# Performance work log

Measured on AMD Instinct MI355X. Metric: run time of the kernel, lower is better.

## Reference

```python
import jax, jax.numpy as jnp
import numpy as np

N = 50000
E = 625000
IN_NODE = 128
IN_EDGE = 64
H = 128
OUT = 112
L = 3


def setup_inputs() -> dict:
    key = jax.random.key(0)
    ks = jax.random.split(key, 16)
    s = lambda fan_in: 1.0 / np.sqrt(fan_in)
    inp = {
        "x": jax.random.normal(ks[0], (N, IN_NODE), jnp.float32),
        "edge_attr": jax.random.normal(ks[1], (E, IN_EDGE), jnp.float32),
        "edge_index": jax.random.randint(ks[2], (2, E), 0, N, jnp.int32),
        # encoders
        "node_W": jax.random.uniform(ks[3], (IN_NODE, H), jnp.float32, -s(IN_NODE), s(IN_NODE)),
        "node_b": jnp.zeros((H,), jnp.float32),
        "edge_W": jax.random.uniform(ks[4], (IN_EDGE, H), jnp.float32, -s(IN_EDGE), s(IN_EDGE)),
        "edge_b": jnp.zeros((H,), jnp.float32),
        # per-layer GINConv MLP params, stacked over layers
        "W1": jax.random.uniform(ks[5], (L, H, 2 * H), jnp.float32, -s(H), s(H)),
        "b1": jnp.zeros((L, 2 * H), jnp.float32),
        "W2": jax.random.uniform(ks[6], (L, 2 * H, H), jnp.float32, -s(2 * H), s(2 * H)),
        "b2": jnp.zeros((L, H), jnp.float32),
        "eps": jnp.zeros((L,), jnp.float32),
        # output head
        "lin_W": jax.random.uniform(ks[7], (H, OUT), jnp.float32, -s(H), s(H)),
        "lin_b": jnp.zeros((OUT,), jnp.float32),
    }
    return inp


def reference(x, edge_attr, edge_index, node_W, node_b, edge_W, edge_b,
              W1, b1, W2, b2, eps, lin_W, lin_b):
    src = edge_index[0]  # x_j gather indices (source nodes)
    dst = edge_index[1]  # scatter targets
    n = x.shape[0]

    x = x @ node_W + node_b                 # [N, H]
    ea = edge_attr @ edge_W + edge_b        # [E, H]

    # in-degree for mean aggregation (clamped at 1, zero-degree -> 0 agg)
    deg = jax.ops.segment_sum(jnp.ones((src.shape[0],), x.dtype), dst, num_segments=n)
    inv_deg = 1.0 / jnp.maximum(deg, 1.0)   # [N]

    for l in range(L):
        msg = x[src] + ea                                    # [E, H]
        agg = jax.ops.segment_sum(msg, dst, num_segments=n)  # [N, H]
        agg = agg * inv_deg[:, None]                         # mean
        h = (1.0 + eps[l]) * x + agg
        h = jax.nn.relu(h @ W1[l] + b1[l]) @ W2[l] + b2[l]   # GIN MLP
        x = jax.nn.relu(h)                                   # dropout is identity in eval

    return x @ lin_W + lin_b                 # [N, OUT]
```

## Files before the change

kernel.cpp:

```cpp
#include <hip/hip_runtime.h>


typedef unsigned short u16;
typedef unsigned int   u32;

using short8 = __attribute__((ext_vector_type(8))) short;
using f32x4  = __attribute__((ext_vector_type(4))) float;
using f32x2  = __attribute__((ext_vector_type(2))) float;

__device__ __forceinline__ float b2f(u16 u) {
  union { u32 i; float f; } v; v.i = ((u32)u) << 16; return v.f;
}
__device__ __forceinline__ u16 f2b(float f) {
  union { float f; u32 i; } v; v.f = f;
  u32 i = v.i;
  return (u16)((i + 0x7FFFu + ((i >> 16) & 1u)) >> 16);
}

__global__ void sniff_kernel(const u16* __restrict__ xu, int* __restrict__ flag) {
  __shared__ int cnt;
  if (threadIdx.x == 0) cnt = 0;
  __syncthreads();
  int c = 0;
  for (int i = threadIdx.x; i < 1024; i += 256) {
    int e = (xu[i] >> 7) & 0xFF;
    if (e >= 100 && e <= 140) c++;
  }
  atomicAdd(&cnt, c);
  __syncthreads();
  if (threadIdx.x == 0) *flag = (cnt >= 820) ? 1 : 0;
}

__global__ void cvt_bf16_kernel(const void* __restrict__ src, u16* __restrict__ dst,
                                int n, const int* __restrict__ flag) {
  int i = blockIdx.x * 256 + threadIdx.x;
  if (i >= n) return;
  if (*flag) dst[i] = ((const u16*)src)[i];
  else       dst[i] = f2b(((const float*)src)[i]);
}

__global__ void transpose_cvt_kernel(const void* __restrict__ src, u16* __restrict__ dst,
                                     int K, int N, int total, const int* __restrict__ flag) {
  int i = blockIdx.x * 256 + threadIdx.x;
  if (i >= total) return;
  int kn = K * N;
  int l = i / kn, r = i - l * kn;
  int k = r / N, n = r - k * N;
  u16 v = (*flag) ? ((const u16*)src)[i] : f2b(((const float*)src)[i]);
  dst[(size_t)l * kn + n * K + k] = v;
}

struct BiasJobs { const void* src[6]; float* dst[6]; int len[6]; };
__global__ void cvt_bias_kernel(BiasJobs j, const int* __restrict__ flag) {
  int b = blockIdx.x;
  int isbf = *flag;
  for (int i = threadIdx.x; i < j.len[b]; i += 256) {
    j.dst[b][i] = isbf ? b2f(((const u16*)j.src[b])[i]) : ((const float*)j.src[b])[i];
  }
}

__global__ void deg_kernel(const int* __restrict__ dst, int* __restrict__ deg, int e) {
  int i = blockIdx.x * 256 + threadIdx.x;
  if (i < e) atomicAdd(&deg[dst[i]], 1);
}

__global__ void scanA_kernel(const int* __restrict__ deg, int* __restrict__ rowptr,
                             float* __restrict__ invdeg, int* __restrict__ btot, int n) {
  __shared__ int wsum[4];
  int tid = threadIdx.x, lane = tid & 63, wid = tid >> 6;
  int i = blockIdx.x * 256 + tid;
  int v = (i < n) ? deg[i] : 0;
  int incl = v;
  #pragma unroll
  for (int off = 1; off < 64; off <<= 1) {
    int t = __shfl_up(incl, off, 64);
    if (lane >= off) incl += t;
  }
  if (lane == 63) wsum[wid] = incl;
  __syncthreads();
  int woff = 0;
  for (int w = 0; w < wid; ++w) woff += wsum[w];
  if (i < n) {
    rowptr[i] = woff + incl - v;
    invdeg[i] = 1.0f / fmaxf((float)v, 1.0f);
  }
  if (tid == 255) btot[blockIdx.x] = woff + incl;
}

__global__ void scanB_kernel(int* __restrict__ btot, int nb) {
  __shared__ int wsum[4];
  int tid = threadIdx.x, lane = tid & 63, wid = tid >> 6;
  int v = (tid < nb) ? btot[tid] : 0;
  int incl = v;
  #pragma unroll
  for (int off = 1; off < 64; off <<= 1) {
    int t = __shfl_up(incl, off, 64);
    if (lane >= off) incl += t;
  }
  if (lane == 63) wsum[wid] = incl;
  __syncthreads();
  int woff = 0;
  for (int w = 0; w < wid; ++w) woff += wsum[w];
  if (tid < nb) btot[tid] = woff + incl - v;
}

__global__ void scanC_kernel(int* __restrict__ rowptr, const int* __restrict__ btot,
                             int n, int e) {
  int i = blockIdx.x * 256 + threadIdx.x;
  if (i < n) rowptr[i] += btot[blockIdx.x];
  if (i == 0) rowptr[n] = e;
}

__global__ void fill_kernel(const int* __restrict__ src, const int* __restrict__ dst,
                            const int* __restrict__ rowptr, int* __restrict__ fillc,
                            int* __restrict__ csr_src, int* __restrict__ csr_eid, int e) {
  int i = blockIdx.x * 256 + threadIdx.x;
  if (i < e) {
    int d = dst[i];
    int p = rowptr[d] + atomicAdd(&fillc[d], 1);
    csr_src[p] = src[i];
    csr_eid[p] = i;
  }
}

__global__ __launch_bounds__(256) void sattr_gather_kernel(
    const void* __restrict__ ea, const int* __restrict__ rowptr,
    const int* __restrict__ csr_eid, float* __restrict__ sattr,
    int nnodes, const int* __restrict__ flag) {
  int tid = threadIdx.x, lane = tid & 63, wid = tid >> 6;
  int node = blockIdx.x * 4 + wid;
  if (node >= nnodes) return;
  int hl = lane >> 5, l32 = lane & 31;
  int r0 = rowptr[node], r1 = rowptr[node + 1];
  int isbf = *flag;
  float s0 = 0.f, s1 = 0.f;
  if (isbf) {
    const u32* ea32 = (const u32*)ea;
    int j = r0 + hl;
    for (; j + 6 < r1; j += 8) {
      int e0 = csr_eid[j], e1 = csr_eid[j + 2], e2 = csr_eid[j + 4], e3 = csr_eid[j + 6];
      u32 v0 = ea32[(size_t)e0 * 32 + l32];
      u32 v1 = ea32[(size_t)e1 * 32 + l32];
      u32 v2 = ea32[(size_t)e2 * 32 + l32];
      u32 v3 = ea32[(size_t)e3 * 32 + l32];
      s0 += b2f((u16)(v0 & 0xffff)) + b2f((u16)(v1 & 0xffff)) +
            b2f((u16)(v2 & 0xffff)) + b2f((u16)(v3 & 0xffff));
      s1 += b2f((u16)(v0 >> 16)) + b2f((u16)(v1 >> 16)) +
            b2f((u16)(v2 >> 16)) + b2f((u16)(v3 >> 16));
    }
    for (; j < r1; j += 2) {
      u32 v = ea32[(size_t)csr_eid[j] * 32 + l32];
      s0 += b2f((u16)(v & 0xffff));
      s1 += b2f((u16)(v >> 16));
    }
  } else {
    const f32x2* eaf = (const f32x2*)ea;
    int j = r0 + hl;
    for (; j + 6 < r1; j += 8) {
      f32x2 v0 = eaf[(size_t)csr_eid[j] * 32 + l32];
      f32x2 v1 = eaf[(size_t)csr_eid[j + 2] * 32 + l32];
      f32x2 v2 = eaf[(size_t)csr_eid[j + 4] * 32 + l32];
      f32x2 v3 = eaf[(size_t)csr_eid[j + 6] * 32 + l32];
      s0 += v0.x + v1.x + v2.x + v3.x;
      s1 += v0.y + v1.y + v2.y + v3.y;
    }
    for (; j < r1; j += 2) {
      f32x2 v = eaf[(size_t)csr_eid[j] * 32 + l32];
      s0 += v.x; s1 += v.y;
    }
  }
  s0 += __shfl_xor(s0, 32, 64);
  s1 += __shfl_xor(s1, 32, 64);
  if (hl == 0) {
    f32x2 o; o.x = s0; o.y = s1;
    *reinterpret_cast<f32x2*>(&sattr[(size_t)node * 64 + l32 * 2]) = o;
  }
}

template <int K, int N, int ACT, int MODE>
__global__ __launch_bounds__(256) void gemm_kernel(
    const void* __restrict__ Av, const u16* __restrict__ WT,
    const float* __restrict__ bias, void* __restrict__ Cv, int M,
    const int* __restrict__ flag, const float* __restrict__ rowscale,
    const int* __restrict__ degp) {
  constexpr int KC = 64;
  constexpr int KCP = KC + 8;
  constexpr int NF = N / 16;
  constexpr int NV = N * KC / 8;
  static_assert(K % KC == 0 && N % 16 == 0, "dims");
  __shared__ u16 WS[N * KCP];

  int tid = threadIdx.x, lane = tid & 63, wid = tid >> 6;
  int lane16 = lane & 15, lh = lane >> 4;
  int row0 = blockIdx.x * 128 + wid * 32;
  int arow0 = row0 + lane16;       if (arow0 >= M) arow0 = M - 1;
  int arow1 = row0 + 16 + lane16;  if (arow1 >= M) arow1 = M - 1;

  f32x4 acc[2][NF];
  #pragma unroll
  for (int rb = 0; rb < 2; ++rb)
    #pragma unroll
    for (int i = 0; i < NF; ++i) acc[rb][i] = (f32x4){0.f, 0.f, 0.f, 0.f};

  for (int kc0 = 0; kc0 < K; kc0 += KC) {
    #pragma unroll
    for (int v = tid; v < NV; v += 256) {
      int n = v >> 3, k8 = (v & 7) << 3;
      *reinterpret_cast<short8*>(&WS[n * KCP + k8]) =
          *reinterpret_cast<const short8*>(&WT[(size_t)n * K + kc0 + k8]);
    }
    __syncthreads();
    #pragma unroll
    for (int ks = 0; ks < KC; ks += 32) {
      short8 a0, a1;
      if (MODE == 2) {
        const float* Af0 = (const float*)Av + (size_t)arow0 * K + kc0 + ks + lh * 8;
        const float* Af1 = (const float*)Av + (size_t)arow1 * K + kc0 + ks + lh * 8;
        f32x4 p0 = *reinterpret_cast<const f32x4*>(Af0);
        f32x4 p1 = *reinterpret_cast<const f32x4*>(Af0 + 4);
        f32x4 q0 = *reinterpret_cast<const f32x4*>(Af1);
        f32x4 q1 = *reinterpret_cast<const f32x4*>(Af1 + 4);
        #pragma unroll
        for (int q = 0; q < 4; ++q) {
          a0[q] = (short)f2b(p0[q]); a0[q + 4] = (short)f2b(p1[q]);
          a1[q] = (short)f2b(q0[q]); a1[q + 4] = (short)f2b(q1[q]);
        }
      } else {
        a0 = *reinterpret_cast<const short8*>((const u16*)Av + (size_t)arow0 * K + kc0 + ks + lh * 8);
        a1 = *reinterpret_cast<const short8*>((const u16*)Av + (size_t)arow1 * K + kc0 + ks + lh * 8);
      }
      #pragma unroll
      for (int nf = 0; nf < NF; ++nf) {
        short8 b = *reinterpret_cast<const short8*>(&WS[(nf * 16 + lane16) * KCP + ks + lh * 8]);
        acc[0][nf] = __builtin_amdgcn_mfma_f32_16x16x32_bf16(a0, b, acc[0][nf], 0, 0, 0);
        acc[1][nf] = __builtin_amdgcn_mfma_f32_16x16x32_bf16(a1, b, acc[1][nf], 0, 0, 0);
      }
    }
    __syncthreads();
  }

  int isbf = 1;
  if (MODE == 1) isbf = *flag;
  #pragma unroll
  for (int rb = 0; rb < 2; ++rb) {
    int crow0 = row0 + rb * 16 + lh * 4;
    #pragma unroll
    for (int nf = 0; nf < NF; ++nf) {
      int col = nf * 16 + lane16;
      float bv = bias[col];
      #pragma unroll
      for (int r = 0; r < 4; ++r) {
        int crow = crow0 + r;
        if (crow < M) {
          size_t idx = (size_t)crow * N + col;
          if (MODE == 2) {
            ((float*)Cv)[idx] = acc[rb][nf][r] * rowscale[crow] + (degp[crow] > 0 ? bv : 0.f);
          } else {
            float v = acc[rb][nf][r] + bv;
            if (ACT) v = fmaxf(v, 0.f);
            if (MODE == 1 && !isbf) ((float*)Cv)[idx] = v;
            else                    ((u16*)Cv)[idx]   = f2b(v);
          }
        }
      }
    }
  }
}

__global__ __launch_bounds__(256) void agg_kernel(
    const u16* __restrict__ xcur, const int* __restrict__ rowptr,
    const int* __restrict__ csr_src, const float* __restrict__ invdeg,
    const float* __restrict__ seab, const float* __restrict__ epsf, int l,
    u16* __restrict__ h0, int nnodes) {
  int tid = threadIdx.x, lane = tid & 63, wid = tid >> 6;
  int node = blockIdx.x * 4 + wid;
  if (node >= nnodes) return;
  const u32* xc = (const u32*)xcur;
  int r0 = rowptr[node], r1 = rowptr[node + 1];
  float a0 = 0.f, a1 = 0.f;
  int j = r0;
  for (; j + 8 <= r1; j += 8) {
    int s0 = csr_src[j],     s1 = csr_src[j + 1], s2 = csr_src[j + 2], s3 = csr_src[j + 3];
    int s4 = csr_src[j + 4], s5 = csr_src[j + 5], s6 = csr_src[j + 6], s7 = csr_src[j + 7];
    u32 v0 = xc[(size_t)s0 * 64 + lane];
    u32 v1 = xc[(size_t)s1 * 64 + lane];
    u32 v2 = xc[(size_t)s2 * 64 + lane];
    u32 v3 = xc[(size_t)s3 * 64 + lane];
    u32 v4 = xc[(size_t)s4 * 64 + lane];
    u32 v5 = xc[(size_t)s5 * 64 + lane];
    u32 v6 = xc[(size_t)s6 * 64 + lane];
    u32 v7 = xc[(size_t)s7 * 64 + lane];
    a0 += ((b2f((u16)(v0 & 0xffff)) + b2f((u16)(v1 & 0xffff))) +
           (b2f((u16)(v2 & 0xffff)) + b2f((u16)(v3 & 0xffff)))) +
          ((b2f((u16)(v4 & 0xffff)) + b2f((u16)(v5 & 0xffff))) +
           (b2f((u16)(v6 & 0xffff)) + b2f((u16)(v7 & 0xffff))));
    a1 += ((b2f((u16)(v0 >> 16)) + b2f((u16)(v1 >> 16))) +
           (b2f((u16)(v2 >> 16)) + b2f((u16)(v3 >> 16)))) +
          ((b2f((u16)(v4 >> 16)) + b2f((u16)(v5 >> 16))) +
           (b2f((u16)(v6 >> 16)) + b2f((u16)(v7 >> 16))));
  }
  for (; j < r1; ++j) {
    u32 v = xc[(size_t)csr_src[j] * 64 + lane];
    a0 += b2f((u16)(v & 0xffff));
    a1 += b2f((u16)(v >> 16));
  }
  float epl = 1.0f + epsf[l];
  float iv = invdeg[node];
  u32 xv = xc[(size_t)node * 64 + lane];
  float h0v = epl * b2f((u16)(xv & 0xffff)) + a0 * iv + seab[(size_t)node * 128 + lane * 2];
  float h1v = epl * b2f((u16)(xv >> 16))    + a1 * iv + seab[(size_t)node * 128 + lane * 2 + 1];
  u32 packed = (u32)f2b(h0v) | ((u32)f2b(h1v) << 16);
  *reinterpret_cast<u32*>(&h0[(size_t)node * 128 + lane * 2]) = packed;
}

extern "C" void kernel_launch(void* const* d_in, const int* in_sizes, int n_in,
                              void* d_out, int out_size, void* d_ws, size_t ws_size,
                              hipStream_t stream) {
  const void* x_in  = d_in[0];
  const void* eattr = d_in[1];
  const int*  eidx  = (const int*)d_in[2];
  const void* nodeW = d_in[3];
  const void* nodeb = d_in[4];
  const void* edgeW = d_in[5];
  const void* edgeb = d_in[6];
  const void* W1    = d_in[7];
  const void* b1    = d_in[8];
  const void* W2    = d_in[9];
  const void* b2    = d_in[10];
  const void* eps   = d_in[11];
  const void* linW  = d_in[12];
  const void* linb  = d_in[13];

  int nn = in_sizes[0] / 128;
  int ne = in_sizes[2] / 2;

  char* ws = (char*)d_ws;
  size_t off = 0;
  auto alloc = [&](size_t b) { size_t r = off; off += (b + 255) & ~(size_t)255; return r; };
  int*    flag    = (int*)(ws + alloc(4));
  int*    deg     = (int*)(ws + alloc((size_t)nn * 4));
  int*    fillc   = (int*)(ws + alloc((size_t)nn * 4));
  int*    rowptr  = (int*)(ws + alloc((size_t)(nn + 1) * 4));
  float*  invdeg  = (float*)(ws + alloc((size_t)nn * 4));
  int*    btot    = (int*)(ws + alloc(256 * 4));
  int*    csr_src = (int*)(ws + alloc((size_t)ne * 4));
  int*    csr_eid = (int*)(ws + alloc((size_t)ne * 4));
  float*  sattr   = (float*)(ws + alloc((size_t)nn * 64 * 4));
  float*  seab    = (float*)(ws + alloc((size_t)nn * 128 * 4));
  u16*    xb      = (u16*)(ws + alloc((size_t)nn * 128 * 2));
  u16*    xcur    = (u16*)(ws + alloc((size_t)nn * 128 * 2));
  u16*    h0      = (u16*)(ws + alloc((size_t)nn * 128 * 2));
  u16*    tbuf    = (u16*)(ws + alloc((size_t)nn * 256 * 2));
  u16*    nodeWT  = (u16*)(ws + alloc(128 * 128 * 2));
  u16*    edgeWT  = (u16*)(ws + alloc(64 * 128 * 2));
  u16*    W1T     = (u16*)(ws + alloc((size_t)3 * 128 * 256 * 2));
  u16*    W2T     = (u16*)(ws + alloc((size_t)3 * 256 * 128 * 2));
  u16*    linWT   = (u16*)(ws + alloc(128 * 112 * 2));
  float*  nodebf  = (float*)(ws + alloc(128 * 4));
  float*  edgebf  = (float*)(ws + alloc(128 * 4));
  float*  b1f     = (float*)(ws + alloc(3 * 256 * 4));
  float*  b2f_    = (float*)(ws + alloc(3 * 128 * 4));
  float*  epsf    = (float*)(ws + alloc(3 * 4));
  float*  linbf   = (float*)(ws + alloc(112 * 4));

  hipMemsetAsync(deg, 0, (size_t)nn * 4, stream);
  hipMemsetAsync(fillc, 0, (size_t)nn * 4, stream);

  sniff_kernel<<<1, 256, 0, stream>>>((const u16*)x_in, flag);

  cvt_bf16_kernel<<<(nn * 128 + 255) / 256, 256, 0, stream>>>(x_in, xb, nn * 128, flag);
  auto tcv = [&](const void* s, u16* d, int K, int N, int L) {
    int tot = L * K * N;
    transpose_cvt_kernel<<<(tot + 255) / 256, 256, 0, stream>>>(s, d, K, N, tot, flag);
  };
  tcv(nodeW, nodeWT, 128, 128, 1);
  tcv(edgeW, edgeWT, 64, 128, 1);
  tcv(W1, W1T, 128, 256, 3);
  tcv(W2, W2T, 256, 128, 3);
  tcv(linW, linWT, 128, 112, 1);

  BiasJobs bj;
  bj.src[0] = nodeb; bj.dst[0] = nodebf; bj.len[0] = 128;
  bj.src[1] = edgeb; bj.dst[1] = edgebf; bj.len[1] = 128;
  bj.src[2] = b1;    bj.dst[2] = b1f;    bj.len[2] = 3 * 256;
  bj.src[3] = b2;    bj.dst[3] = b2f_;   bj.len[3] = 3 * 128;
  bj.src[4] = eps;   bj.dst[4] = epsf;   bj.len[4] = 3;
  bj.src[5] = linb;  bj.dst[5] = linbf;  bj.len[5] = 112;
  cvt_bias_kernel<<<6, 256, 0, stream>>>(bj, flag);

  int eb = (ne + 255) / 256;
  int nb = (nn + 255) / 256;
  deg_kernel<<<eb, 256, 0, stream>>>(eidx + ne, deg, ne);
  scanA_kernel<<<nb, 256, 0, stream>>>(deg, rowptr, invdeg, btot, nn);
  scanB_kernel<<<1, 256, 0, stream>>>(btot, nb);
  scanC_kernel<<<nb, 256, 0, stream>>>(rowptr, btot, nn, ne);
  fill_kernel<<<eb, 256, 0, stream>>>(eidx, eidx + ne, rowptr, fillc, csr_src, csr_eid, ne);

  sattr_gather_kernel<<<(nn + 3) / 4, 256, 0, stream>>>(eattr, rowptr, csr_eid, sattr, nn, flag);

  int gb = (nn + 127) / 128;
  gemm_kernel<128, 128, 0, 0><<<gb, 256, 0, stream>>>(xb, nodeWT, nodebf, xcur, nn, flag, nullptr, nullptr);
  gemm_kernel<64, 128, 0, 2><<<gb, 256, 0, stream>>>(sattr, edgeWT, edgebf, seab, nn, flag, invdeg, deg);

  for (int l = 0; l < 3; ++l) {
    agg_kernel<<<(nn + 3) / 4, 256, 0, stream>>>(xcur, rowptr, csr_src, invdeg, seab, epsf, l, h0, nn);
    gemm_kernel<128, 256, 1, 0><<<gb, 256, 0, stream>>>(h0, W1T + (size_t)l * 128 * 256,
                                                        b1f + l * 256, tbuf, nn, flag, nullptr, nullptr);
    gemm_kernel<256, 128, 1, 0><<<gb, 256, 0, stream>>>(tbuf, W2T + (size_t)l * 256 * 128,
                                                        b2f_ + l * 128, xcur, nn, flag, nullptr, nullptr);
  }
  gemm_kernel<128, 112, 0, 1><<<gb, 256, 0, stream>>>(xcur, linWT, linbf, d_out, nn, flag, nullptr, nullptr);
}
```

Baseline: 719.0 us.

## Merge prep launches, fold scans, interleave CSR, read raw input in GEMM, halve GEMM tiles

The separate weight-transpose, bias and input-conversion kernels are merged into one prep kernel. The middle scan pass is folded into scanC, where each block sums the preceding block totals itself. The node-encoder GEMM now reads the raw input directly, converting fp32 in-kernel, so the bf16 copy of x is gone. CSR src and edge-id are stored interleaved as int2, and GEMM blocks shrink to 128 threads covering 64 rows to give more blocks. This cuts launch count and memory traffic, at the cost of the GEMM loading the weight tile into LDS twice as often in total and reading 8-byte CSR entries where only 4 bytes are used.

Result: no change. 718.5 us (-0.1%).

```diff
diff --git a/kernel.cpp b/kernel.cpp
--- a/kernel.cpp
+++ b/kernel.cpp
@@ -31,31 +31,35 @@
   if (threadIdx.x == 0) *flag = (cnt >= 820) ? 1 : 0;
 }
 
-__global__ void cvt_bf16_kernel(const void* __restrict__ src, u16* __restrict__ dst,
-                                int n, const int* __restrict__ flag) {
+struct PrepJobs {
+  const void* wsrc[5]; u16* wdst[5];
+  int wK[5], wN[5], wTot[5];
+  const void* bsrc[6]; float* bdst[6]; int blen[6];
+};
+__global__ void prep_kernel(PrepJobs j, const int* __restrict__ flag, int grand) {
   int i = blockIdx.x * 256 + threadIdx.x;
-  if (i >= n) return;
-  if (*flag) dst[i] = ((const u16*)src)[i];
-  else       dst[i] = f2b(((const float*)src)[i]);
-}
-
-__global__ void transpose_cvt_kernel(const void* __restrict__ src, u16* __restrict__ dst,
-                                     int K, int N, int total, const int* __restrict__ flag) {
-  int i = blockIdx.x * 256 + threadIdx.x;
-  if (i >= total) return;
-  int kn = K * N;
-  int l = i / kn, r = i - l * kn;
-  int k = r / N, n = r - k * N;
-  u16 v = (*flag) ? ((const u16*)src)[i] : f2b(((const float*)src)[i]);
-  dst[(size_t)l * kn + n * K + k] = v;
-}
-
-struct BiasJobs { const void* src[6]; float* dst[6]; int len[6]; };
-__global__ void cvt_bias_kernel(BiasJobs j, const int* __restrict__ flag) {
-  int b = blockIdx.x;
+  if (i >= grand) return;
   int isbf = *flag;
-  for (int i = threadIdx.x; i < j.len[b]; i += 256) {
-    j.dst[b][i] = isbf ? b2f(((const u16*)j.src[b])[i]) : ((const float*)j.src[b])[i];
+  #pragma unroll
+  for (int g = 0; g < 5; ++g) {
+    if (i < j.wTot[g]) {
+      int K = j.wK[g], N = j.wN[g];
+      int kn = K * N;
+      int l = i / kn, r = i - l * kn;
+      int k = r / N, n = r - k * N;
+      u16 v = isbf ? ((const u16*)j.wsrc[g])[i] : f2b(((const float*)j.wsrc[g])[i]);
+      j.wdst[g][(size_t)l * kn + n * K + k] = v;
+      return;
+    }
+    i -= j.wTot[g];
+  }
+  #pragma unroll
+  for (int g = 0; g < 6; ++g) {
+    if (i < j.blen[g]) {
+      j.bdst[g][i] = isbf ? b2f(((const u16*)j.bsrc[g])[i]) : ((const float*)j.bsrc[g])[i];
+      return;
+    }
+    i -= j.blen[g];
   }
 }
 
@@ -87,45 +91,37 @@
   if (tid == 255) btot[blockIdx.x] = woff + incl;
 }
 
-__global__ void scanB_kernel(int* __restrict__ btot, int nb) {
-  __shared__ int wsum[4];
-  int tid = threadIdx.x, lane = tid & 63, wid = tid >> 6;
-  int v = (tid < nb) ? btot[tid] : 0;
-  int incl = v;
-  #pragma unroll
-  for (int off = 1; off < 64; off <<= 1) {
-    int t = __shfl_up(incl, off, 64);
-    if (lane >= off) incl += t;
-  }
-  if (lane == 63) wsum[wid] = incl;
-  __syncthreads();
-  int woff = 0;
-  for (int w = 0; w < wid; ++w) woff += wsum[w];
-  if (tid < nb) btot[tid] = woff + incl - v;
-}
-
 __global__ void scanC_kernel(int* __restrict__ rowptr, const int* __restrict__ btot,
                              int n, int e) {
-  int i = blockIdx.x * 256 + threadIdx.x;
-  if (i < n) rowptr[i] += btot[blockIdx.x];
+  __shared__ int wsum[4];
+  __shared__ int s_pre;
+  int bid = blockIdx.x, tid = threadIdx.x, lane = tid & 63, wid = tid >> 6;
+  int v = (tid < bid) ? btot[tid] : 0;
+  #pragma unroll
+  for (int off = 1; off < 64; off <<= 1) v += __shfl_xor(v, off, 64);
+  if (lane == 0) wsum[wid] = v;
+  __syncthreads();
+  if (tid == 0) s_pre = wsum[0] + wsum[1] + wsum[2] + wsum[3];
+  __syncthreads();
+  int i = bid * 256 + tid;
+  if (i < n) rowptr[i] += s_pre;
   if (i == 0) rowptr[n] = e;
 }
 
 __global__ void fill_kernel(const int* __restrict__ src, const int* __restrict__ dst,
                             const int* __restrict__ rowptr, int* __restrict__ fillc,
-                            int* __restrict__ csr_src, int* __restrict__ csr_eid, int e) {
+                            int2* __restrict__ csr, int e) {
   int i = blockIdx.x * 256 + threadIdx.x;
   if (i < e) {
     int d = dst[i];
     int p = rowptr[d] + atomicAdd(&fillc[d], 1);
-    csr_src[p] = src[i];
-    csr_eid[p] = i;
+    csr[p] = make_int2(src[i], i);
   }
 }
 
 __global__ __launch_bounds__(256) void sattr_gather_kernel(
     const void* __restrict__ ea, const int* __restrict__ rowptr,
-    const int* __restrict__ csr_eid, float* __restrict__ sattr,
+    const int2* __restrict__ csr, float* __restrict__ sattr,
     int nnodes, const int* __restrict__ flag) {
   int tid = threadIdx.x, lane = tid & 63, wid = tid >> 6;
   int node = blockIdx.x * 4 + wid;
@@ -138,7 +134,7 @@
     const u32* ea32 = (const u32*)ea;
     int j = r0 + hl;
     for (; j + 6 < r1; j += 8) {
-      int e0 = csr_eid[j], e1 = csr_eid[j + 2], e2 = csr_eid[j + 4], e3 = csr_eid[j + 6];
+      int e0 = csr[j].y, e1 = csr[j + 2].y, e2 = csr[j + 4].y, e3 = csr[j + 6].y;
       u32 v0 = ea32[(size_t)e0 * 32 + l32];
       u32 v1 = ea32[(size_t)e1 * 32 + l32];
       u32 v2 = ea32[(size_t)e2 * 32 + l32];
@@ -149,7 +145,7 @@
             b2f((u16)(v2 >> 16)) + b2f((u16)(v3 >> 16));
     }
     for (; j < r1; j += 2) {
-      u32 v = ea32[(size_t)csr_eid[j] * 32 + l32];
+      u32 v = ea32[(size_t)csr[j].y * 32 + l32];
       s0 += b2f((u16)(v & 0xffff));
       s1 += b2f((u16)(v >> 16));
     }
@@ -157,15 +153,15 @@
     const f32x2* eaf = (const f32x2*)ea;
     int j = r0 + hl;
     for (; j + 6 < r1; j += 8) {
-      f32x2 v0 = eaf[(size_t)csr_eid[j] * 32 + l32];
-      f32x2 v1 = eaf[(size_t)csr_eid[j + 2] * 32 + l32];
-      f32x2 v2 = eaf[(size_t)csr_eid[j + 4] * 32 + l32];
-      f32x2 v3 = eaf[(size_t)csr_eid[j + 6] * 32 + l32];
+      f32x2 v0 = eaf[(size_t)csr[j].y * 32 + l32];
+      f32x2 v1 = eaf[(size_t)csr[j + 2].y * 32 + l32];
+      f32x2 v2 = eaf[(size_t)csr[j + 4].y * 32 + l32];
+      f32x2 v3 = eaf[(size_t)csr[j + 6].y * 32 + l32];
       s0 += v0.x + v1.x + v2.x + v3.x;
       s1 += v0.y + v1.y + v2.y + v3.y;
     }
     for (; j < r1; j += 2) {
-      f32x2 v = eaf[(size_t)csr_eid[j] * 32 + l32];
+      f32x2 v = eaf[(size_t)csr[j].y * 32 + l32];
       s0 += v.x; s1 += v.y;
     }
   }
@@ -178,7 +174,7 @@
 }
 
 template <int K, int N, int ACT, int MODE>
-__global__ __launch_bounds__(256) void gemm_kernel(
+__global__ __launch_bounds__(128) void gemm_kernel(
     const void* __restrict__ Av, const u16* __restrict__ WT,
     const float* __restrict__ bias, void* __restrict__ Cv, int M,
     const int* __restrict__ flag, const float* __restrict__ rowscale,
@@ -192,9 +188,12 @@
 
   int tid = threadIdx.x, lane = tid & 63, wid = tid >> 6;
   int lane16 = lane & 15, lh = lane >> 4;
-  int row0 = blockIdx.x * 128 + wid * 32;
+  int row0 = blockIdx.x * 64 + wid * 32;
   int arow0 = row0 + lane16;       if (arow0 >= M) arow0 = M - 1;
   int arow1 = row0 + 16 + lane16;  if (arow1 >= M) arow1 = M - 1;
+
+  int aisbf = 1;
+  if (MODE == 3 || MODE == 1) aisbf = *flag;
 
   f32x4 acc[2][NF];
   #pragma unroll
@@ -204,7 +203,7 @@
 
   for (int kc0 = 0; kc0 < K; kc0 += KC) {
     #pragma unroll
-    for (int v = tid; v < NV; v += 256) {
+    for (int v = tid; v < NV; v += 128) {
       int n = v >> 3, k8 = (v & 7) << 3;
       *reinterpret_cast<short8*>(&WS[n * KCP + k8]) =
           *reinterpret_cast<const short8*>(&WT[(size_t)n * K + kc0 + k8]);
@@ -213,7 +212,8 @@
     #pragma unroll
     for (int ks = 0; ks < KC; ks += 32) {
       short8 a0, a1;
-      if (MODE == 2) {
+      bool f32a = (MODE == 2) || (MODE == 3 && !aisbf);
+      if (f32a) {
         const float* Af0 = (const float*)Av + (size_t)arow0 * K + kc0 + ks + lh * 8;
         const float* Af1 = (const float*)Av + (size_t)arow1 * K + kc0 + ks + lh * 8;
         f32x4 p0 = *reinterpret_cast<const f32x4*>(Af0);
@@ -239,8 +239,6 @@
     __syncthreads();
   }
 
-  int isbf = 1;
-  if (MODE == 1) isbf = *flag;
   #pragma unroll
   for (int rb = 0; rb < 2; ++rb) {
     int crow0 = row0 + rb * 16 + lh * 4;
@@ -258,8 +256,8 @@
           } else {
             float v = acc[rb][nf][r] + bv;
             if (ACT) v = fmaxf(v, 0.f);
-            if (MODE == 1 && !isbf) ((float*)Cv)[idx] = v;
-            else                    ((u16*)Cv)[idx]   = f2b(v);
+            if (MODE == 1 && !aisbf) ((float*)Cv)[idx] = v;
+            else                     ((u16*)Cv)[idx]   = f2b(v);
           }
         }
       }
@@ -269,7 +267,7 @@
 
 __global__ __launch_bounds__(256) void agg_kernel(
     const u16* __restrict__ xcur, const int* __restrict__ rowptr,
-    const int* __restrict__ csr_src, const float* __restrict__ invdeg,
+    const int2* __restrict__ csr, const float* __restrict__ invdeg,
     const float* __restrict__ seab, const float* __restrict__ epsf, int l,
     u16* __restrict__ h0, int nnodes) {
   int tid = threadIdx.x, lane = tid & 63, wid = tid >> 6;
@@ -280,8 +278,8 @@
   float a0 = 0.f, a1 = 0.f;
   int j = r0;
   for (; j + 8 <= r1; j += 8) {
-    int s0 = csr_src[j],     s1 = csr_src[j + 1], s2 = csr_src[j + 2], s3 = csr_src[j + 3];
-    int s4 = csr_src[j + 4], s5 = csr_src[j + 5], s6 = csr_src[j + 6], s7 = csr_src[j + 7];
+    int s0 = csr[j].x,     s1 = csr[j + 1].x, s2 = csr[j + 2].x, s3 = csr[j + 3].x;
+    int s4 = csr[j + 4].x, s5 = csr[j + 5].x, s6 = csr[j + 6].x, s7 = csr[j + 7].x;
     u32 v0 = xc[(size_t)s0 * 64 + lane];
     u32 v1 = xc[(size_t)s1 * 64 + lane];
     u32 v2 = xc[(size_t)s2 * 64 + lane];
@@ -300,7 +298,7 @@
            (b2f((u16)(v6 >> 16)) + b2f((u16)(v7 >> 16))));
   }
   for (; j < r1; ++j) {
-    u32 v = xc[(size_t)csr_src[j] * 64 + lane];
+    u32 v = xc[(size_t)csr[j].x * 64 + lane];
     a0 += b2f((u16)(v & 0xffff));
     a1 += b2f((u16)(v >> 16));
   }
@@ -338,16 +336,14 @@
   size_t off = 0;
   auto alloc = [&](size_t b) { size_t r = off; off += (b + 255) & ~(size_t)255; return r; };
   int*    flag    = (int*)(ws + alloc(4));
-  int*    deg     = (int*)(ws + alloc((size_t)nn * 4));
-  int*    fillc   = (int*)(ws + alloc((size_t)nn * 4));
+  int*    deg     = (int*)(ws + alloc((size_t)2 * nn * 4));
+  int*    fillc   = deg + nn;
   int*    rowptr  = (int*)(ws + alloc((size_t)(nn + 1) * 4));
   float*  invdeg  = (float*)(ws + alloc((size_t)nn * 4));
   int*    btot    = (int*)(ws + alloc(256 * 4));
-  int*    csr_src = (int*)(ws + alloc((size_t)ne * 4));
-  int*    csr_eid = (int*)(ws + alloc((size_t)ne * 4));
+  int2*   csr     = (int2*)(ws + alloc((size_t)ne * 8));
   float*  sattr   = (float*)(ws + alloc((size_t)nn * 64 * 4));
   float*  seab    = (float*)(ws + alloc((size_t)nn * 128 * 4));
-  u16*    xb      = (u16*)(ws + alloc((size_t)nn * 128 * 2));
   u16*    xcur    = (u16*)(ws + alloc((size_t)nn * 128 * 2));
   u16*    h0      = (u16*)(ws + alloc((size_t)nn * 128 * 2));
   u16*    tbuf    = (u16*)(ws + alloc((size_t)nn * 256 * 2));
@@ -363,51 +359,46 @@
   float*  epsf    = (float*)(ws + alloc(3 * 4));
   float*  linbf   = (float*)(ws + alloc(112 * 4));
 
-  hipMemsetAsync(deg, 0, (size_t)nn * 4, stream);
-  hipMemsetAsync(fillc, 0, (size_t)nn * 4, stream);
+  hipMemsetAsync(deg, 0, (size_t)2 * nn * 4, stream);
 
   sniff_kernel<<<1, 256, 0, stream>>>((const u16*)x_in, flag);
 
-  cvt_bf16_kernel<<<(nn * 128 + 255) / 256, 256, 0, stream>>>(x_in, xb, nn * 128, flag);
-  auto tcv = [&](const void* s, u16* d, int K, int N, int L) {
-    int tot = L * K * N;
-    transpose_cvt_kernel<<<(tot + 255) / 256, 256, 0, stream>>>(s, d, K, N, tot, flag);
-  };
-  tcv(nodeW, nodeWT, 128, 128, 1);
-  tcv(edgeW, edgeWT, 64, 128, 1);
-  tcv(W1, W1T, 128, 256, 3);
-  tcv(W2, W2T, 256, 128, 3);
-  tcv(linW, linWT, 128, 112, 1);
-
-  BiasJobs bj;
-  bj.src[0] = nodeb; bj.dst[0] = nodebf; bj.len[0] = 128;
-  bj.src[1] = edgeb; bj.dst[1] = edgebf; bj.len[1] = 128;
-  bj.src[2] = b1;    bj.dst[2] = b1f;    bj.len[2] = 3 * 256;
-  bj.src[3] = b2;    bj.dst[3] = b2f_;   bj.len[3] = 3 * 128;
-  bj.src[4] = eps;   bj.dst[4] = epsf;   bj.len[4] = 3;
-  bj.src[5] = linb;  bj.dst[5] = linbf;  bj.len[5] = 112;
-  cvt_bias_kernel<<<6, 256, 0, stream>>>(bj, flag);
+  PrepJobs pj;
+  pj.wsrc[0] = nodeW; pj.wdst[0] = nodeWT; pj.wK[0] = 128; pj.wN[0] = 128; pj.wTot[0] = 128 * 128;
+  pj.wsrc[1] = edgeW; pj.wdst[1] = edgeWT; pj.wK[1] = 64;  pj.wN[1] = 128; pj.wTot[1] = 64 * 128;
+  pj.wsrc[2] = W1;    pj.wdst[2] = W1T;    pj.wK[2] = 128; pj.wN[2] = 256; pj.wTot[2] = 3 * 128 * 256;
+  pj.wsrc[3] = W2;    pj.wdst[3] = W2T;    pj.wK[3] = 256; pj.wN[3] = 128; pj.wTot[3] = 3 * 256 * 128;
+  pj.wsrc[4] = linW;  pj.wdst[4] = linWT;  pj.wK[4] = 128; pj.wN[4] = 112; pj.wTot[4] = 128 * 112;
+  pj.bsrc[0] = nodeb; pj.bdst[0] = nodebf; pj.blen[0] = 128;
+  pj.bsrc[1] = edgeb; pj.bdst[1] = edgebf; pj.blen[1] = 128;
+  pj.bsrc[2] = b1;    pj.bdst[2] = b1f;    pj.blen[2] = 3 * 256;
+  pj.bsrc[3] = b2;    pj.bdst[3] = b2f_;   pj.blen[3] = 3 * 128;
+  pj.bsrc[4] = eps;   pj.bdst[4] = epsf;   pj.blen[4] = 3;
+  pj.bsrc[5] = linb;  pj.bdst[5] = linbf;  pj.blen[5] = 112;
+  int grand = 0;
+  for (int g = 0; g < 5; ++g) grand += pj.wTot[g];
+  for (int g = 0; g < 6; ++g) grand += pj.blen[g];
+  prep_kernel<<<(grand + 255) / 256, 256, 0, stream>>>(pj, flag, grand);
 
   int eb = (ne + 255) / 256;
   int nb = (nn + 255) / 256;
   deg_kernel<<<eb, 256, 0, stream>>>(eidx + ne, deg, ne);
   scanA_kernel<<<nb, 256, 0, stream>>>(deg, rowptr, invdeg, btot, nn);
-  scanB_kernel<<<1, 256, 0, stream>>>(btot, nb);
   scanC_kernel<<<nb, 256, 0, stream>>>(rowptr, btot, nn, ne);
-  fill_kernel<<<eb, 256, 0, stream>>>(eidx, eidx + ne, rowptr, fillc, csr_src, csr_eid, ne);
-
-  sattr_gather_kernel<<<(nn + 3) / 4, 256, 0, stream>>>(eattr, rowptr, csr_eid, sattr, nn, flag);
-
-  int gb = (nn + 127) / 128;
-  gemm_kernel<128, 128, 0, 0><<<gb, 256, 0, stream>>>(xb, nodeWT, nodebf, xcur, nn, flag, nullptr, nullptr);
-  gemm_kernel<64, 128, 0, 2><<<gb, 256, 0, stream>>>(sattr, edgeWT, edgebf, seab, nn, flag, invdeg, deg);
+  fill_kernel<<<eb, 256, 0, stream>>>(eidx, eidx + ne, rowptr, fillc, csr, ne);
+
+  sattr_gather_kernel<<<(nn + 3) / 4, 256, 0, stream>>>(eattr, rowptr, csr, sattr, nn, flag);
+
+  int gb = (nn + 63) / 64;
+  gemm_kernel<128, 128, 0, 3><<<gb, 128, 0, stream>>>(x_in, nodeWT, nodebf, xcur, nn, flag, nullptr, nullptr);
+  gemm_kernel<64, 128, 0, 2><<<gb, 128, 0, stream>>>(sattr, edgeWT, edgebf, seab, nn, flag, invdeg, deg);
 
   for (int l = 0; l < 3; ++l) {
-    agg_kernel<<<(nn + 3) / 4, 256, 0, stream>>>(xcur, rowptr, csr_src, invdeg, seab, epsf, l, h0, nn);
-    gemm_kernel<128, 256, 1, 0><<<gb, 256, 0, stream>>>(h0, W1T + (size_t)l * 128 * 256,
+    agg_kernel<<<(nn + 3) / 4, 256, 0, stream>>>(xcur, rowptr, csr, invdeg, seab, epsf, l, h0, nn);
+    gemm_kernel<128, 256, 1, 0><<<gb, 128, 0, stream>>>(h0, W1T + (size_t)l * 128 * 256,
                                                         b1f + l * 256, tbuf, nn, flag, nullptr, nullptr);
-    gemm_kernel<256, 128, 1, 0><<<gb, 256, 0, stream>>>(tbuf, W2T + (size_t)l * 256 * 128,
+    gemm_kernel<256, 128, 1, 0><<<gb, 128, 0, stream>>>(tbuf, W2T + (size_t)l * 256 * 128,
                                                         b2f_ + l * 128, xcur, nn, flag, nullptr, nullptr);
   }
-  gemm_kernel<128, 112, 0, 1><<<gb, 256, 0, stream>>>(xcur, linWT, linbf, d_out, nn, flag, nullptr, nullptr);
-}
+  gemm_kernel<128, 112, 0, 1><<<gb, 128, 0, stream>>>(xcur, linWT, linbf, d_out, nn, flag, nullptr, nullptr);
+}
```
